# Optimization experiments

Hardware: AMD Instinct MI355X
Metric: run time of the kernel (lower is better)

Reference implementation:

```python
import jax, jax.numpy as jnp
import numpy as np

IN_DIM, HIDDEN, CLASSES, NBASIS = 1024, 4096, 1000, 16

def setup_inputs() -> dict:
    key = jax.random.key(0)
    ks = jax.random.split(key, 7)
    x = jax.random.normal(ks[0], (4096, IN_DIM), dtype=jnp.float32)
    # FerroelectricBasis params: per-feature tanh basis (centers, scales) + dense mix
    centers = jax.random.normal(ks[1], (IN_DIM, NBASIS), dtype=jnp.float32)
    scales = jax.random.uniform(ks[2], (IN_DIM, NBASIS), dtype=jnp.float32, minval=0.5, maxval=2.0)
    s = 1.0 / np.sqrt(IN_DIM * NBASIS)
    Wb = jax.random.uniform(ks[3], (IN_DIM * NBASIS, HIDDEN), dtype=jnp.float32, minval=-s, maxval=s)
    bb = jax.random.uniform(ks[4], (HIDDEN,), dtype=jnp.float32, minval=-s, maxval=s)
    sh = 1.0 / np.sqrt(HIDDEN)
    Wh = jax.random.uniform(ks[5], (HIDDEN, CLASSES), dtype=jnp.float32, minval=-sh, maxval=sh)
    bh = jax.random.uniform(ks[6], (CLASSES,), dtype=jnp.float32, minval=-sh, maxval=sh)
    return {"x": x, "centers": centers, "scales": scales, "Wb": Wb, "bb": bb, "Wh": Wh, "bh": bh}

def reference(x, centers, scales, Wb, bb, Wh, bh):
    B = x.shape[0]
    # ferroelectric (hysteresis-like) tanh basis expansion: [B, in_dim, num_basis]
    feats = jnp.tanh((x[:, :, None] - centers[None]) * scales[None])
    feats = feats.reshape(B, -1)                      # [B, in_dim*num_basis]
    h = feats @ Wb + bb                               # [B, hidden]
    phi = jax.nn.sigmoid(h)
    logits = phi @ Wh + bh                            # [B, num_classes]
    return logits
```

## Files before the change

kernel.cpp:

```cpp
#include <hip/hip_runtime.h>
#include <hip/hip_bf16.h>

typedef __bf16 bf16x8_t __attribute__((ext_vector_type(8)));
typedef float f32x4_t __attribute__((ext_vector_type(4)));
typedef int i32x4_t __attribute__((ext_vector_type(4)));
typedef int i32x8_t __attribute__((ext_vector_type(8)));

#define GLDS(gp, lp) __builtin_amdgcn_global_load_lds(                        \
    (const __attribute__((address_space(1))) void*)(gp),                      \
    (__attribute__((address_space(3))) void*)(lp), 16, 0, 0)

__device__ __forceinline__ float fast_tanh(float z) {
  float zc = fminf(10.0f, fmaxf(-10.0f, z));
  float e = __expf(2.0f * zc);
  return 1.0f - 2.0f / (e + 1.0f);
}

__device__ __forceinline__ int pack_fp8x4(float a, float b, float c, float d) {
  int w = __builtin_amdgcn_cvt_pk_fp8_f32(a, b, 0, false);
  w = __builtin_amdgcn_cvt_pk_fp8_f32(c, d, w, true);
  return w;
}

__global__ __launch_bounds__(256) void feats_kernel(
    const float* __restrict__ x, const float* __restrict__ c,
    const float* __restrict__ s, unsigned char* __restrict__ out) {
  int idx = blockIdx.x * 256 + threadIdx.x;
  int d = idx & 1023;
  float xv = x[idx];
  const float4* c4 = (const float4*)(c + d * 16);
  const float4* s4 = (const float4*)(s + d * 16);
  int w[4];
#pragma unroll
  for (int g = 0; g < 4; ++g) {
    float4 cc = c4[g], ss = s4[g];
    float t0 = fast_tanh((xv - cc.x) * ss.x);
    float t1 = fast_tanh((xv - cc.y) * ss.y);
    float t2 = fast_tanh((xv - cc.z) * ss.z);
    float t3 = fast_tanh((xv - cc.w) * ss.w);
    w[g] = pack_fp8x4(t0, t1, t2, t3);
  }
  *(uint4*)(out + (size_t)idx * 16) = make_uint4(w[0], w[1], w[2], w[3]);
}

__global__ __launch_bounds__(256) void transpose_fp8(
    const float* __restrict__ src, unsigned char* __restrict__ dst, int R, int C) {
  __shared__ float tile[64][65];
  const int c0 = blockIdx.x * 64, r0 = blockIdx.y * 64;
  const int t = threadIdx.x;
  const int rr = t >> 4, cc4 = (t & 15) * 4;
#pragma unroll
  for (int p = 0; p < 4; ++p) {
    int row = rr + p * 16;
    float4 v = *(const float4*)(src + (size_t)(r0 + row) * C + c0 + cc4);
    tile[row][cc4 + 0] = v.x;
    tile[row][cc4 + 1] = v.y;
    tile[row][cc4 + 2] = v.z;
    tile[row][cc4 + 3] = v.w;
  }
  __syncthreads();
  const int drow = t >> 2, seg = (t & 3) * 16;
  int w[4];
#pragma unroll
  for (int g = 0; g < 4; ++g) {
    float a = tile[seg + g * 4 + 0][drow] * 128.0f;
    float b = tile[seg + g * 4 + 1][drow] * 128.0f;
    float cc = tile[seg + g * 4 + 2][drow] * 128.0f;
    float d = tile[seg + g * 4 + 3][drow] * 128.0f;
    w[g] = pack_fp8x4(a, b, cc, d);
  }
  *(uint4*)(dst + (size_t)(c0 + drow) * R + r0 + seg) = make_uint4(w[0], w[1], w[2], w[3]);
}

__global__ __launch_bounds__(256) void transpose_cast(
    const float* __restrict__ src, __hip_bfloat16* __restrict__ dst,
    int R, int C, int Cpad) {
  __shared__ float tile[64][65];
  const int c0 = blockIdx.x * 64, r0 = blockIdx.y * 64;
  const int t = threadIdx.x;
  const int rr = t >> 4, cc4 = (t & 15) * 4;
#pragma unroll
  for (int p = 0; p < 4; ++p) {
    int row = rr + p * 16;
    int cbase = c0 + cc4;
    float4 v;
    if (cbase + 3 < C) {
      v = *(const float4*)(src + (size_t)(r0 + row) * C + cbase);
    } else {
      v.x = (cbase + 0 < C) ? src[(size_t)(r0 + row) * C + cbase + 0] : 0.0f;
      v.y = (cbase + 1 < C) ? src[(size_t)(r0 + row) * C + cbase + 1] : 0.0f;
      v.z = (cbase + 2 < C) ? src[(size_t)(r0 + row) * C + cbase + 2] : 0.0f;
      v.w = (cbase + 3 < C) ? src[(size_t)(r0 + row) * C + cbase + 3] : 0.0f;
    }
    tile[row][cc4 + 0] = v.x;
    tile[row][cc4 + 1] = v.y;
    tile[row][cc4 + 2] = v.z;
    tile[row][cc4 + 3] = v.w;
  }
  __syncthreads();
#pragma unroll
  for (int p = 0; p < 2; ++p) {
    int i = t + 256 * p;
    int drow = i >> 3;
    int seg = (i & 7) * 8;
    int dc = c0 + drow;
    alignas(16) __hip_bfloat16 vals[8];
#pragma unroll
    for (int j = 0; j < 8; ++j) vals[j] = __float2bfloat16(tile[seg + j][drow]);
    if (dc < Cpad)
      *(uint4*)(dst + (size_t)dc * R + r0 + seg) = *(const uint4*)vals;
  }
}

__global__ __launch_bounds__(256) void gemm1_mx(
    const unsigned char* __restrict__ A, const unsigned char* __restrict__ Bt,
    const float* __restrict__ bias, __hip_bfloat16* __restrict__ outb,
    int M, int N, int K) {
  __shared__ unsigned char As[128 * 128];
  __shared__ unsigned char Bs[128 * 128];
  const int tid = threadIdx.x;
  const int wave = tid >> 6, lane = tid & 63;
  const int wm = (wave >> 1) * 64, wn = (wave & 1) * 64;
  const int gm0 = blockIdx.y * 128, gn0 = blockIdx.x * 128;

  const unsigned char* ga[4];
  const unsigned char* gb[4];
  int ldso[4];
#pragma unroll
  for (int p = 0; p < 4; ++p) {
    int cch = p * 256 + tid;
    int row = cch >> 3;
    int g = (cch & 7) ^ (row & 7);
    ga[p] = A + (size_t)(gm0 + row) * K + g * 16;
    gb[p] = Bt + (size_t)(gn0 + row) * K + g * 16;
    ldso[p] = cch * 16;
  }

  f32x4_t acc[4][4] = {};
  const int fr = lane & 15, kh = lane >> 4;

  for (int k0 = 0; k0 < K; k0 += 128) {
#pragma unroll
    for (int p = 0; p < 4; ++p) {
      GLDS(ga[p] + k0, As + ldso[p]);
      GLDS(gb[p] + k0, Bs + ldso[p]);
    }
    __syncthreads();
    i32x8_t a[4], b[4];
#pragma unroll
    for (int i = 0; i < 4; ++i) {
      int ra = wm + i * 16 + fr, sa = ra & 7;
      i32x4_t alo = *(const i32x4_t*)(As + ra * 128 + (((2 * kh) ^ sa) * 16));
      i32x4_t ahi = *(const i32x4_t*)(As + ra * 128 + (((2 * kh + 1) ^ sa) * 16));
      a[i] = __builtin_shufflevector(alo, ahi, 0, 1, 2, 3, 4, 5, 6, 7);
      int rb = wn + i * 16 + fr, sb = rb & 7;
      i32x4_t blo = *(const i32x4_t*)(Bs + rb * 128 + (((2 * kh) ^ sb) * 16));
      i32x4_t bhi = *(const i32x4_t*)(Bs + rb * 128 + (((2 * kh + 1) ^ sb) * 16));
      b[i] = __builtin_shufflevector(blo, bhi, 0, 1, 2, 3, 4, 5, 6, 7);
    }
#pragma unroll
    for (int i = 0; i < 4; ++i)
#pragma unroll
      for (int j = 0; j < 4; ++j)
        acc[i][j] = __builtin_amdgcn_mfma_scale_f32_16x16x128_f8f6f4(
            a[i], b[j], acc[i][j], 0, 0, 0, 0x7F7F7F7F, 0, 0x7F7F7F7F);
    __syncthreads();
  }

  const int cn = lane & 15, cm = (lane >> 4) * 4;
#pragma unroll
  for (int j = 0; j < 4; ++j) {
    int n = gn0 + wn + j * 16 + cn;
    float bv = bias[n];
#pragma unroll
    for (int i = 0; i < 4; ++i) {
#pragma unroll
      for (int r = 0; r < 4; ++r) {
        int m = gm0 + wm + i * 16 + cm + r;
        float v = acc[i][j][r] * 0.0078125f + bv;
        float phi = 1.0f / (1.0f + __expf(-v));
        outb[(size_t)m * N + n] = __float2bfloat16(phi);
      }
    }
  }
}

__global__ __launch_bounds__(256) void gemm2_bt(
    const __hip_bfloat16* __restrict__ A, const __hip_bfloat16* __restrict__ Bt,
    float* __restrict__ outf, int M, int N, int K, int kcount) {
  __shared__ __hip_bfloat16 As[2][128 * 32];
  __shared__ __hip_bfloat16 Bs[2][128 * 32];
  const int tid = threadIdx.x;
  const int wave = tid >> 6, lane = tid & 63;
  const int wm = (wave >> 1) * 64, wn = (wave & 1) * 64;
  const int gm0 = blockIdx.y * 128, gn0 = blockIdx.x * 128;
  const int kbeg = blockIdx.z * kcount;

  const int t1 = tid, t2 = tid + 256;
  const __hip_bfloat16* Ag0 = A + (size_t)(gm0 + (t1 >> 2)) * K + kbeg + (t1 & 3) * 8;
  const __hip_bfloat16* Ag1 = A + (size_t)(gm0 + (t2 >> 2)) * K + kbeg + (t2 & 3) * 8;
  const __hip_bfloat16* Bg0 = Bt + (size_t)(gn0 + (t1 >> 2)) * K + kbeg + (t1 & 3) * 8;
  const __hip_bfloat16* Bg1 = Bt + (size_t)(gn0 + (t2 >> 2)) * K + kbeg + (t2 & 3) * 8;

  f32x4_t acc[4][4] = {};
  const int fr = lane & 15, fk = (lane >> 4) * 8;

  for (int k0 = 0; k0 < kcount; k0 += 64) {
#pragma unroll
    for (int h = 0; h < 2; ++h) {
      GLDS(Ag0 + h * 32, &As[h][t1 * 8]);
      GLDS(Ag1 + h * 32, &As[h][t2 * 8]);
      GLDS(Bg0 + h * 32, &Bs[h][t1 * 8]);
      GLDS(Bg1 + h * 32, &Bs[h][t2 * 8]);
    }
    Ag0 += 64; Ag1 += 64; Bg0 += 64; Bg1 += 64;
    __syncthreads();
#pragma unroll
    for (int h = 0; h < 2; ++h) {
      bf16x8_t a[4], b[4];
#pragma unroll
      for (int i = 0; i < 4; ++i) {
        a[i] = *(const bf16x8_t*)(&As[h][(wm + i * 16 + fr) * 32 + fk]);
        b[i] = *(const bf16x8_t*)(&Bs[h][(wn + i * 16 + fr) * 32 + fk]);
      }
#pragma unroll
      for (int i = 0; i < 4; ++i)
#pragma unroll
        for (int j = 0; j < 4; ++j)
          acc[i][j] = __builtin_amdgcn_mfma_f32_16x16x32_bf16(a[i], b[j], acc[i][j], 0, 0, 0);
    }
    __syncthreads();
  }

  const int cn = lane & 15, cm = (lane >> 4) * 4;
#pragma unroll
  for (int j = 0; j < 4; ++j) {
    int n = gn0 + wn + j * 16 + cn;
#pragma unroll
    for (int i = 0; i < 4; ++i)
#pragma unroll
      for (int r = 0; r < 4; ++r) {
        int m = gm0 + wm + i * 16 + cm + r;
        outf[((size_t)blockIdx.z * M + m) * N + n] = acc[i][j][r];
      }
  }
}

__global__ __launch_bounds__(256) void reduce4_kernel(
    const float* __restrict__ p, const float* __restrict__ bh,
    float* __restrict__ out) {
  int n = blockIdx.x * 256 + threadIdx.x;
  int m = blockIdx.y;
  const size_t zs = (size_t)4096 * 1024;
  if (n < 1000) {
    size_t o = (size_t)m * 1024 + n;
    out[(size_t)m * 1000 + n] = p[o] + p[zs + o] + p[2 * zs + o] + p[3 * zs + o] + bh[n];
  }
}

extern "C" void kernel_launch(void* const* d_in, const int* in_sizes, int n_in,
                              void* d_out, int out_size, void* d_ws, size_t ws_size,
                              hipStream_t stream) {
  const float* x = (const float*)d_in[0];
  const float* centers = (const float*)d_in[1];
  const float* scales = (const float*)d_in[2];
  const float* Wb = (const float*)d_in[3];
  const float* bb = (const float*)d_in[4];
  const float* Wh = (const float*)d_in[5];
  const float* bh = (const float*)d_in[6];
  float* out = (float*)d_out;

  unsigned char* feats = (unsigned char*)d_ws;
  unsigned char* Wbt = feats + (size_t)4096 * 16384;
  __hip_bfloat16* phi = (__hip_bfloat16*)(Wbt + (size_t)4096 * 16384);
  __hip_bfloat16* Wht = phi + (size_t)4096 * 4096;
  float* partial = (float*)d_ws;

  feats_kernel<<<dim3(16384), dim3(256), 0, stream>>>(x, centers, scales, feats);
  transpose_fp8<<<dim3(64, 256), dim3(256), 0, stream>>>(Wb, Wbt, 16384, 4096);
  transpose_cast<<<dim3(16, 64), dim3(256), 0, stream>>>(Wh, Wht, 4096, 1000, 1024);
  gemm1_mx<<<dim3(32, 32), dim3(256), 0, stream>>>(feats, Wbt, bb, phi, 4096, 4096, 16384);
  gemm2_bt<<<dim3(8, 32, 4), dim3(256), 0, stream>>>(phi, Wht, partial, 4096, 1024, 4096, 1024);
  reduce4_kernel<<<dim3(4, 4096), dim3(256), 0, stream>>>(partial, bh, out);
}
```

Measured before the change: 861.8 us.

## Restructure FP8 GEMM1 into 256x256 tiles with double-buffered LDS and swizzled blocks

Replaces the 128x128 single-buffered MX-FP8 GEMM with a 512-thread 256x256 tile kernel. It double-buffers LDS so the next K slice is fetched with global_load_lds while the current slice is computed, interleaves those async loads with MFMA groups, and raises MFMA wave priority. Block IDs are remapped into grouped tiles to improve L2 reuse of A and B, and the larger tile gives more reuse per byte loaded. The cost is 128KB of LDS and higher register pressure from 32 accumulators per thread, which limit occupancy, and only 256 blocks are launched.

After: 773.8 us. 1.11x faster.

```diff
diff --git a/kernel.cpp b/kernel.cpp
--- a/kernel.cpp
+++ b/kernel.cpp
@@ -112,58 +112,94 @@
   }
 }
 
-__global__ __launch_bounds__(256) void gemm1_mx(
+__global__ __launch_bounds__(512, 2) void gemm1_mx8(
     const unsigned char* __restrict__ A, const unsigned char* __restrict__ Bt,
     const float* __restrict__ bias, __hip_bfloat16* __restrict__ outb,
     int M, int N, int K) {
-  __shared__ unsigned char As[128 * 128];
-  __shared__ unsigned char Bs[128 * 128];
+  __shared__ unsigned char As[2][256 * 128];
+  __shared__ unsigned char Bs[2][256 * 128];
   const int tid = threadIdx.x;
   const int wave = tid >> 6, lane = tid & 63;
-  const int wm = (wave >> 1) * 64, wn = (wave & 1) * 64;
-  const int gm0 = blockIdx.y * 128, gn0 = blockIdx.x * 128;
+  const int wm = (wave >> 2) * 128, wn = (wave & 3) * 64;
+
+  const int bid = blockIdx.x;
+  const int swz = (bid & 7) * 32 + (bid >> 3);
+  const int gq = swz >> 5, u = swz & 31;
+  const int gm0 = ((gq >> 1) * 4 + (u >> 3)) * 256;
+  const int gn0 = ((gq & 1) * 8 + (u & 7)) * 256;
 
   const unsigned char* ga[4];
   const unsigned char* gb[4];
   int ldso[4];
 #pragma unroll
   for (int p = 0; p < 4; ++p) {
-    int cch = p * 256 + tid;
-    int row = cch >> 3;
-    int g = (cch & 7) ^ (row & 7);
+    int c = p * 512 + tid;
+    int row = c >> 3;
+    int g = (c & 7) ^ (row & 7);
     ga[p] = A + (size_t)(gm0 + row) * K + g * 16;
     gb[p] = Bt + (size_t)(gn0 + row) * K + g * 16;
-    ldso[p] = cch * 16;
-  }
-
-  f32x4_t acc[4][4] = {};
+    ldso[p] = c * 16;
+  }
+
+  f32x4_t acc[8][4] = {};
   const int fr = lane & 15, kh = lane >> 4;
 
-  for (int k0 = 0; k0 < K; k0 += 128) {
+#pragma unroll
+  for (int p = 0; p < 4; ++p) {
+    GLDS(ga[p], &As[0][ldso[p]]);
+    GLDS(gb[p], &Bs[0][ldso[p]]);
+  }
+  __syncthreads();
+
+  const int NT = K >> 7;
+  for (int t = 0; t < NT; ++t) {
+    const unsigned char* Ac = As[t & 1];
+    const unsigned char* Bc = Bs[t & 1];
+    unsigned char* An = (unsigned char*)As[(t + 1) & 1];
+    unsigned char* Bn = (unsigned char*)Bs[(t + 1) & 1];
+    const int k1 = (t + 1) << 7;
+    const bool pre = (t + 1 < NT);
+
+    i32x8_t b[4];
+#pragma unroll
+    for (int j = 0; j < 4; ++j) {
+      int rb = wn + j * 16 + fr, sb = rb & 7;
+      i32x4_t blo = *(const i32x4_t*)(Bc + rb * 128 + (((2 * kh) ^ sb) * 16));
+      i32x4_t bhi = *(const i32x4_t*)(Bc + rb * 128 + (((2 * kh + 1) ^ sb) * 16));
+      b[j] = __builtin_shufflevector(blo, bhi, 0, 1, 2, 3, 4, 5, 6, 7);
+    }
+
 #pragma unroll
     for (int p = 0; p < 4; ++p) {
-      GLDS(ga[p] + k0, As + ldso[p]);
-      GLDS(gb[p] + k0, Bs + ldso[p]);
-    }
-    __syncthreads();
-    i32x8_t a[4], b[4];
-#pragma unroll
-    for (int i = 0; i < 4; ++i) {
-      int ra = wm + i * 16 + fr, sa = ra & 7;
-      i32x4_t alo = *(const i32x4_t*)(As + ra * 128 + (((2 * kh) ^ sa) * 16));
-      i32x4_t ahi = *(const i32x4_t*)(As + ra * 128 + (((2 * kh + 1) ^ sa) * 16));
-      a[i] = __builtin_shufflevector(alo, ahi, 0, 1, 2, 3, 4, 5, 6, 7);
-      int rb = wn + i * 16 + fr, sb = rb & 7;
-      i32x4_t blo = *(const i32x4_t*)(Bs + rb * 128 + (((2 * kh) ^ sb) * 16));
-      i32x4_t bhi = *(const i32x4_t*)(Bs + rb * 128 + (((2 * kh + 1) ^ sb) * 16));
-      b[i] = __builtin_shufflevector(blo, bhi, 0, 1, 2, 3, 4, 5, 6, 7);
-    }
-#pragma unroll
-    for (int i = 0; i < 4; ++i)
-#pragma unroll
-      for (int j = 0; j < 4; ++j)
-        acc[i][j] = __builtin_amdgcn_mfma_scale_f32_16x16x128_f8f6f4(
-            a[i], b[j], acc[i][j], 0, 0, 0, 0x7F7F7F7F, 0, 0x7F7F7F7F);
+      if (pre) {
+        GLDS(ga[p] + k1, An + ldso[p]);
+        GLDS(gb[p] + k1, Bn + ldso[p]);
+      }
+      i32x8_t a0, a1;
+      {
+        int ra = wm + (2 * p + 0) * 16 + fr, sa = ra & 7;
+        i32x4_t lo = *(const i32x4_t*)(Ac + ra * 128 + (((2 * kh) ^ sa) * 16));
+        i32x4_t hi = *(const i32x4_t*)(Ac + ra * 128 + (((2 * kh + 1) ^ sa) * 16));
+        a0 = __builtin_shufflevector(lo, hi, 0, 1, 2, 3, 4, 5, 6, 7);
+      }
+      {
+        int ra = wm + (2 * p + 1) * 16 + fr, sa = ra & 7;
+        i32x4_t lo = *(const i32x4_t*)(Ac + ra * 128 + (((2 * kh) ^ sa) * 16));
+        i32x4_t hi = *(const i32x4_t*)(Ac + ra * 128 + (((2 * kh + 1) ^ sa) * 16));
+        a1 = __builtin_shufflevector(lo, hi, 0, 1, 2, 3, 4, 5, 6, 7);
+      }
+      __builtin_amdgcn_s_barrier();
+      __builtin_amdgcn_s_setprio(1);
+#pragma unroll
+      for (int j = 0; j < 4; ++j) {
+        acc[2 * p + 0][j] = __builtin_amdgcn_mfma_scale_f32_16x16x128_f8f6f4(
+            a0, b[j], acc[2 * p + 0][j], 0, 0, 0, 0x7F7F7F7F, 0, 0x7F7F7F7F);
+        acc[2 * p + 1][j] = __builtin_amdgcn_mfma_scale_f32_16x16x128_f8f6f4(
+            a1, b[j], acc[2 * p + 1][j], 0, 0, 0, 0x7F7F7F7F, 0, 0x7F7F7F7F);
+      }
+      __builtin_amdgcn_s_setprio(0);
+      if (p < 3) __builtin_amdgcn_s_barrier();
+    }
     __syncthreads();
   }
 
@@ -173,7 +209,7 @@
     int n = gn0 + wn + j * 16 + cn;
     float bv = bias[n];
 #pragma unroll
-    for (int i = 0; i < 4; ++i) {
+    for (int i = 0; i < 8; ++i) {
 #pragma unroll
       for (int r = 0; r < 4; ++r) {
         int m = gm0 + wm + i * 16 + cm + r;
@@ -279,7 +315,7 @@
   feats_kernel<<<dim3(16384), dim3(256), 0, stream>>>(x, centers, scales, feats);
   transpose_fp8<<<dim3(64, 256), dim3(256), 0, stream>>>(Wb, Wbt, 16384, 4096);
   transpose_cast<<<dim3(16, 64), dim3(256), 0, stream>>>(Wh, Wht, 4096, 1000, 1024);
-  gemm1_mx<<<dim3(32, 32), dim3(256), 0, stream>>>(feats, Wbt, bb, phi, 4096, 4096, 16384);
+  gemm1_mx8<<<dim3(256), dim3(512), 0, stream>>>(feats, Wbt, bb, phi, 4096, 4096, 16384);
   gemm2_bt<<<dim3(8, 32, 4), dim3(256), 0, stream>>>(phi, Wht, partial, 4096, 1024, 4096, 1024);
   reduce4_kernel<<<dim3(4, 4096), dim3(256), 0, stream>>>(partial, bh, out);
 }
```
